# Performance work log

Measured on AMD Instinct MI355X. Metric: run time of the kernel, lower is better.

## Reference

```python
import jax, jax.numpy as jnp
import numpy as np

EMB = 1024
HEADS = 16
HEAD_DIM = EMB // HEADS


def setup_inputs() -> dict:
    key = jax.random.key(0)
    k1, k2, k3, k4 = jax.random.split(key, 4)
    x = jax.random.normal(k1, (4, 2048, EMB), dtype=jnp.float32)
    # torch Linear weight is [out, in]; store as [in, out] for x @ W
    W_qkv = jax.random.normal(k2, (EMB, 3 * EMB), dtype=jnp.float32) * (1.0 / np.sqrt(EMB))
    W_proj = jax.random.normal(k3, (EMB, EMB), dtype=jnp.float32) * (1.0 / np.sqrt(EMB))
    b_proj = jax.random.normal(k4, (EMB,), dtype=jnp.float32) * 0.01
    return {"x": x, "W_qkv": W_qkv, "W_proj": W_proj, "b_proj": b_proj}


def reference(x, W_qkv, W_proj, b_proj):
    B, S, D = x.shape
    H, hd = HEADS, HEAD_DIM
    qkv = x @ W_qkv                                  # [B,S,3D]
    q, k, v = jnp.split(qkv, 3, axis=-1)
    q = q.reshape(B, S, H, hd).transpose(0, 2, 1, 3)  # [B,H,S,hd]
    k = k.reshape(B, S, H, hd).transpose(0, 2, 1, 3)
    v = v.reshape(B, S, H, hd).transpose(0, 2, 1, 3)
    att = jnp.einsum('bhqd,bhkd->bhqk', q, k) * (1.0 / np.sqrt(hd))
    causal = jnp.tril(jnp.ones((S, S), dtype=bool))
    att = jnp.where(causal[None, None], att, jnp.float32(-jnp.inf))
    att = jax.nn.softmax(att, axis=-1)
    # dropout omitted (eval mode / deterministic baseline)
    out = jnp.einsum('bhqk,bhkd->bhqd', att, v)       # [B,H,S,hd]
    out = out.transpose(0, 2, 1, 3).reshape(B, S, D)
    return out @ W_proj + b_proj
```

## Files before the change

### kernel.cpp

```cpp
#include <hip/hip_runtime.h>
#include <math.h>

#define S_   2048
#define D_   1024
#define H_   16
#define HD_  64
#define BH_  64
#define TOK_ 8192

typedef __attribute__((ext_vector_type(8))) short  short8;
typedef __attribute__((ext_vector_type(4))) float  floatx4;

__device__ __forceinline__ short f2bf(float f) {
  union { float f; unsigned u; } c; c.f = f;
  unsigned u = c.u;
  u += 0x7fffu + ((u >> 16) & 1u);
  return (short)(u >> 16);
}

__device__ __forceinline__ float max3f(float a, float b, float c) {
  float d; asm("v_max3_f32 %0, %1, %2, %3" : "=v"(d) : "v"(a), "v"(b), "v"(c)); return d;
}

__device__ __forceinline__ void gload16(const void* g, void* l) {
  __builtin_amdgcn_global_load_lds((const __attribute__((address_space(1))) void*)g,
                                   (__attribute__((address_space(3))) void*)l, 16, 0, 0);
}

__global__ void cvt_x_kernel(const float* __restrict__ in, short* __restrict__ out, int n8) {
  int i = blockIdx.x * blockDim.x + threadIdx.x;
  if (i >= n8) return;
  const float4* p = (const float4*)in;
  float4 a = p[i * 2], b = p[i * 2 + 1];
  short8 o;
  o[0] = f2bf(a.x); o[1] = f2bf(a.y); o[2] = f2bf(a.z); o[3] = f2bf(a.w);
  o[4] = f2bf(b.x); o[5] = f2bf(b.y); o[6] = f2bf(b.z); o[7] = f2bf(b.w);
  ((short8*)out)[i] = o;
}

__global__ void tconv_kernel(const float* __restrict__ in, short* __restrict__ out, int R, int C) {
  __shared__ float t[32][33];
  int tx = threadIdx.x, ty = threadIdx.y;
  int c0 = blockIdx.x * 32, r0 = blockIdx.y * 32;
#pragma unroll
  for (int i = 0; i < 4; ++i)
    t[ty + i * 8][tx] = in[(r0 + ty + i * 8) * C + c0 + tx];
  __syncthreads();
#pragma unroll
  for (int i = 0; i < 4; ++i)
    out[(c0 + ty + i * 8) * R + r0 + tx] = f2bf(t[tx][ty + i * 8]);
}

__global__ __launch_bounds__(256) void gemm_qkv_kernel(
    const short* __restrict__ A, const short* __restrict__ Bt,
    short* __restrict__ qb, short* __restrict__ kb, short* __restrict__ vtb) {
  __shared__ short sA[128 * 32];
  __shared__ short sB[128 * 32];
  const int tid = threadIdx.x;
  const int lane = tid & 63, wid = tid >> 6;
  const int wm = wid >> 1, wn = wid & 1;
  const int lr = lane & 15, lg = lane >> 4;
  const int m0 = blockIdx.x * 128, n0 = blockIdx.y * 128;
  floatx4 acc[4][4] = {};
  const int f1 = tid * 16;
  const int rS1 = f1 >> 6, cS1 = (f1 & 63) >> 1;
  const int f2 = f1 + 4096;
  const int rS2 = f2 >> 6, cS2 = (f2 & 63) >> 1;
  for (int kt = 0; kt < 32; ++kt) {
    const int k0 = kt * 32;
    __syncthreads();
    gload16(&A[(m0 + rS1) * 1024 + k0 + cS1], (char*)sA + f1);
    gload16(&A[(m0 + rS2) * 1024 + k0 + cS2], (char*)sA + f2);
    gload16(&Bt[(n0 + rS1) * 1024 + k0 + cS1], (char*)sB + f1);
    gload16(&Bt[(n0 + rS2) * 1024 + k0 + cS2], (char*)sB + f2);
    __syncthreads();
    short8 af[4], bfv[4];
#pragma unroll
    for (int mf = 0; mf < 4; ++mf)
      af[mf] = *(const short8*)&sA[(wm * 64 + mf * 16 + lr) * 32 + lg * 8];
#pragma unroll
    for (int nf = 0; nf < 4; ++nf)
      bfv[nf] = *(const short8*)&sB[(wn * 64 + nf * 16 + lr) * 32 + lg * 8];
#pragma unroll
    for (int mf = 0; mf < 4; ++mf)
#pragma unroll
      for (int nf = 0; nf < 4; ++nf)
        acc[mf][nf] = __builtin_amdgcn_mfma_f32_16x16x32_bf16(af[mf], bfv[nf], acc[mf][nf], 0, 0, 0);
  }
  const int sec = n0 >> 10;
  if (sec < 2) {
    short* dst = sec == 0 ? qb : kb;
    const float scale = (sec == 0) ? 0.18033688011112042f : 1.0f;
#pragma unroll
    for (int mf = 0; mf < 4; ++mf) {
#pragma unroll
      for (int nf = 0; nf < 4; ++nf) {
        const int col = n0 + wn * 64 + nf * 16 + lr;
        const int w = col & 1023;
        const int h = w >> 6, d = w & 63;
#pragma unroll
        for (int r = 0; r < 4; ++r) {
          const int token = m0 + wm * 64 + mf * 16 + lg * 4 + r;
          const int b = token >> 11, s = token & 2047;
          dst[(((b << 4) | h) * 2048 + s) * 64 + d] = f2bf(acc[mf][nf][r] * scale);
        }
      }
    }
  } else {
#pragma unroll
    for (int mf = 0; mf < 4; ++mf) {
      const int token0 = m0 + wm * 64 + mf * 16 + lg * 4;
      const int bb = token0 >> 11, s0v = token0 & 2047;
#pragma unroll
      for (int nf = 0; nf < 4; ++nf) {
        const int col = n0 + wn * 64 + nf * 16 + lr;
        const int w = col & 1023;
        const int h = w >> 6, d = w & 63;
        union { unsigned long long u; short s[4]; } pk;
        pk.s[0] = f2bf(acc[mf][nf][0]);
        pk.s[1] = f2bf(acc[mf][nf][1]);
        pk.s[2] = f2bf(acc[mf][nf][2]);
        pk.s[3] = f2bf(acc[mf][nf][3]);
        *(unsigned long long*)&vtb[((((bb << 4) | h) * 64 + d) << 11) + s0v] = pk.u;
      }
    }
  }
}

__global__ __launch_bounds__(256) void gemm_proj_kernel(
    const short* __restrict__ A, const short* __restrict__ Bt,
    const float* __restrict__ bias, float* __restrict__ out) {
  __shared__ short sA[128 * 32];
  __shared__ short sB[128 * 32];
  const int tid = threadIdx.x;
  const int lane = tid & 63, wid = tid >> 6;
  const int wm = wid >> 1, wn = wid & 1;
  const int lr = lane & 15, lg = lane >> 4;
  const int m0 = blockIdx.x * 128, n0 = blockIdx.y * 128;
  floatx4 acc[4][4] = {};
  const int f1 = tid * 16;
  const int rS1 = f1 >> 6, cS1 = (f1 & 63) >> 1;
  const int f2 = f1 + 4096;
  const int rS2 = f2 >> 6, cS2 = (f2 & 63) >> 1;
  for (int kt = 0; kt < 32; ++kt) {
    const int k0 = kt * 32;
    __syncthreads();
    gload16(&A[(m0 + rS1) * 1024 + k0 + cS1], (char*)sA + f1);
    gload16(&A[(m0 + rS2) * 1024 + k0 + cS2], (char*)sA + f2);
    gload16(&Bt[(n0 + rS1) * 1024 + k0 + cS1], (char*)sB + f1);
    gload16(&Bt[(n0 + rS2) * 1024 + k0 + cS2], (char*)sB + f2);
    __syncthreads();
    short8 af[4], bfv[4];
#pragma unroll
    for (int mf = 0; mf < 4; ++mf)
      af[mf] = *(const short8*)&sA[(wm * 64 + mf * 16 + lr) * 32 + lg * 8];
#pragma unroll
    for (int nf = 0; nf < 4; ++nf)
      bfv[nf] = *(const short8*)&sB[(wn * 64 + nf * 16 + lr) * 32 + lg * 8];
#pragma unroll
    for (int mf = 0; mf < 4; ++mf)
#pragma unroll
      for (int nf = 0; nf < 4; ++nf)
        acc[mf][nf] = __builtin_amdgcn_mfma_f32_16x16x32_bf16(af[mf], bfv[nf], acc[mf][nf], 0, 0, 0);
  }
#pragma unroll
  for (int mf = 0; mf < 4; ++mf) {
#pragma unroll
    for (int nf = 0; nf < 4; ++nf) {
      const int col = n0 + wn * 64 + nf * 16 + lr;
      const float bv = bias[col];
#pragma unroll
      for (int r = 0; r < 4; ++r) {
        const int row = m0 + wm * 64 + mf * 16 + lg * 4 + r;
        out[row * 1024 + col] = acc[mf][nf][r] + bv;
      }
    }
  }
}

__global__ __launch_bounds__(256) void attn_kernel(
    const short* __restrict__ qb, const short* __restrict__ kb,
    const short* __restrict__ vtb, short* __restrict__ attb) {
  __shared__ short sK[3][64 * 64];
  __shared__ short sVT[3][64 * 64];
  __shared__ short sP[4][32 * 64];
  const int tid = threadIdx.x;
  const int lane = tid & 63, wid = tid >> 6;
  const int lr = lane & 15, lg = lane >> 4;

  const int bid = blockIdx.x;
  const int wgid = (bid & 7) * 64 + (bid >> 3);
  const int bh = wgid >> 3;
  const int qx = wgid & 7;

  const char* kbase = (const char*)(kb + bh * S_ * HD_);
  const char* vtbase = (const char*)(vtb + bh * HD_ * S_);
  const short* qbase = qb + bh * S_ * HD_;
  char* pbase = (char*)&sP[wid][0];
  const int b = bh >> 4, h = bh & 15;

  const int f1 = tid * 16;
  const int ro1 = f1 >> 7, cb1 = f1 & 127;
  const int sc1 = cb1 ^ ((ro1 & 7) << 4);
  const int f2 = f1 + 4096;
  const int ro2 = f2 >> 7, cb2 = f2 & 127;
  const int sc2 = cb2 ^ ((ro2 & 7) << 4);

  const int swz = (lr & 7) << 4;

  short8 vones;
#pragma unroll
  for (int j = 0; j < 8; ++j) vones[j] = (short)0x3F80;

#pragma unroll 1
  for (int half = 0; half < 2; ++half) {
    const int qt = half ? (15 - qx) : qx;
    const int qw = qt * 128 + wid * 32;

    short8 qf[2][2];
#pragma unroll
    for (int qtile = 0; qtile < 2; ++qtile)
#pragma unroll
      for (int kf = 0; kf < 2; ++kf)
        qf[qtile][kf] = *(const short8*)&qbase[(qw + qtile * 16 + lr) * 64 + kf * 32 + lg * 8];

    floatx4 acc_o[2][4] = {};
    floatx4 acc_den[2] = {};
    float mrun[2] = {-1e30f, -1e30f};

    const int ntiles = 2 * qt + 2;

    __builtin_amdgcn_s_barrier();

    const char* kp1 = kbase + ro1 * 128 + sc1;
    const char* kp2 = kbase + ro2 * 128 + sc2;
    const char* vp1 = vtbase + ro1 * 4096 + sc1;
    const char* vp2 = vtbase + ro2 * 4096 + sc2;

    gload16(kp1, (char*)sK[0] + f1);  gload16(kp2, (char*)sK[0] + f2);
    gload16(vp1, (char*)sVT[0] + f1); gload16(vp2, (char*)sVT[0] + f2);
    kp1 += 8192; kp2 += 8192; vp1 += 128; vp2 += 128;
    gload16(kp1, (char*)sK[1] + f1);  gload16(kp2, (char*)sK[1] + f2);
    gload16(vp1, (char*)sVT[1] + f1); gload16(vp2, (char*)sVT[1] + f2);
    kp1 += 8192; kp2 += 8192; vp1 += 128; vp2 += 128;

    int cur = 0, nxt2 = 2;
#pragma unroll 1
    for (int t = 0; t < ntiles; ++t) {
      if (t < ntiles - 1) { asm volatile("s_waitcnt vmcnt(4)" ::: "memory"); }
      else                { asm volatile("s_waitcnt vmcnt(0)" ::: "memory"); }
      __builtin_amdgcn_s_barrier();
      __builtin_amdgcn_sched_barrier(0);
      if (t + 2 < ntiles) {
        char* dK = (char*)sK[nxt2];
        char* dV = (char*)sVT[nxt2];
        gload16(kp1, dK + f1);  gload16(kp2, dK + f2);
        gload16(vp1, dV + f1);  gload16(vp2, dV + f2);
      }
      kp1 += 8192; kp2 += 8192; vp1 += 128; vp2 += 128;

      const int key0 = t * 64;
      if (key0 <= qw + 31) {
        const char* cK = (const char*)sK[cur];
        const char* cV = (const char*)sVT[cur];

        floatx4 sT[4][2] = {};
        __builtin_amdgcn_s_setprio(1);
#pragma unroll
        for (int kt = 0; kt < 4; ++kt) {
#pragma unroll
          for (int kf = 0; kf < 2; ++kf) {
            short8 kfrag = *(const short8*)(cK + (kt * 16 + lr) * 128 + ((kf * 64 + lg * 16) ^ swz));
#pragma unroll
            for (int qtile = 0; qtile < 2; ++qtile)
              sT[kt][qtile] = __builtin_amdgcn_mfma_f32_16x16x32_bf16(kfrag, qf[qtile][kf], sT[kt][qtile], 0, 0, 0);
          }
        }
        __builtin_amdgcn_s_setprio(0);

        if (key0 + 63 > qw) {
#pragma unroll
          for (int kt = 0; kt < 4; ++kt)
#pragma unroll
            for (int qtile = 0; qtile < 2; ++qtile)
#pragma unroll
              for (int r = 0; r < 4; ++r)
                if (key0 + kt * 16 + lg * 4 + r > qw + qtile * 16 + lr) sT[kt][qtile][r] = -1e30f;
        }

        float mx[2], al[2];
        bool need = false;
#pragma unroll
        for (int qtile = 0; qtile < 2; ++qtile) {
          float m = max3f(sT[0][qtile][0], sT[0][qtile][1], sT[0][qtile][2]);
          m = max3f(m, sT[0][qtile][3], sT[1][qtile][0]);
          m = max3f(m, sT[1][qtile][1], sT[1][qtile][2]);
          m = max3f(m, sT[1][qtile][3], sT[2][qtile][0]);
          m = max3f(m, sT[2][qtile][1], sT[2][qtile][2]);
          m = max3f(m, sT[2][qtile][3], sT[3][qtile][0]);
          m = max3f(m, sT[3][qtile][1], sT[3][qtile][2]);
          m = fmaxf(m, sT[3][qtile][3]);
          m = fmaxf(m, __shfl_xor(m, 16));
          m = fmaxf(m, __shfl_xor(m, 32));
          mx[qtile] = m;
          need = need || (m > mrun[qtile] + 8.f);
        }
        if (__any(need)) {
#pragma unroll
          for (int qtile = 0; qtile < 2; ++qtile) {
            const float mnew = fmaxf(mrun[qtile], mx[qtile]);
            al[qtile] = __builtin_amdgcn_exp2f(mrun[qtile] - mnew);
            mrun[qtile] = mnew;
          }
#pragma unroll
          for (int mf = 0; mf < 2; ++mf) {
#pragma unroll
            for (int r = 0; r < 4; ++r) {
              const float alr = __shfl(al[mf], lg * 4 + r);
              acc_den[mf][r] *= alr;
#pragma unroll
              for (int nfd = 0; nfd < 4; ++nfd) acc_o[mf][nfd][r] *= alr;
            }
          }
        }

#pragma unroll
        for (int kt = 0; kt < 4; ++kt) {
#pragma unroll
          for (int qtile = 0; qtile < 2; ++qtile) {
            const float p0 = __builtin_amdgcn_exp2f(sT[kt][qtile][0] - mrun[qtile]);
            const float p1 = __builtin_amdgcn_exp2f(sT[kt][qtile][1] - mrun[qtile]);
            const float p2 = __builtin_amdgcn_exp2f(sT[kt][qtile][2] - mrun[qtile]);
            const float p3 = __builtin_amdgcn_exp2f(sT[kt][qtile][3] - mrun[qtile]);
            unsigned lo, hi;
            asm("v_cvt_pk_bf16_f32 %0, %1, %2" : "=v"(lo) : "v"(p0), "v"(p1));
            asm("v_cvt_pk_bf16_f32 %0, %1, %2" : "=v"(hi) : "v"(p2), "v"(p3));
            *(unsigned long long*)(pbase + (qtile * 16 + lr) * 128 + ((kt * 32 + lg * 8) ^ swz)) =
                ((unsigned long long)hi << 32) | lo;
          }
        }

        __builtin_amdgcn_s_setprio(1);
#pragma unroll
        for (int kf2 = 0; kf2 < 2; ++kf2) {
          short8 pf[2];
#pragma unroll
          for (int mf = 0; mf < 2; ++mf) {
            pf[mf] = *(const short8*)(pbase + (mf * 16 + lr) * 128 + ((kf2 * 64 + lg * 16) ^ swz));
            acc_den[mf] = __builtin_amdgcn_mfma_f32_16x16x32_bf16(pf[mf], vones, acc_den[mf], 0, 0, 0);
          }
#pragma unroll
          for (int nfd = 0; nfd < 4; ++nfd) {
            short8 vfrag = *(const short8*)(cV + (nfd * 16 + lr) * 128 + ((kf2 * 64 + lg * 16) ^ swz));
#pragma unroll
            for (int mf = 0; mf < 2; ++mf)
              acc_o[mf][nfd] = __builtin_amdgcn_mfma_f32_16x16x32_bf16(pf[mf], vfrag, acc_o[mf][nfd], 0, 0, 0);
          }
        }
        __builtin_amdgcn_s_setprio(0);
      }

      cur = (cur == 2) ? 0 : cur + 1;
      nxt2 = (nxt2 == 2) ? 0 : nxt2 + 1;
    }

#pragma unroll
    for (int mf = 0; mf < 2; ++mf) {
#pragma unroll
      for (int nfd = 0; nfd < 4; ++nfd) {
#pragma unroll
        for (int r = 0; r < 4; ++r) {
          const float o = acc_o[mf][nfd][r] / acc_den[mf][r];
          const int qrow = qw + mf * 16 + lg * 4 + r;
          const int d = nfd * 16 + lr;
          attb[(b * 2048 + qrow) * 1024 + h * 64 + d] = f2bf(o);
        }
      }
    }
  }
}

extern "C" void kernel_launch(void* const* d_in, const int* in_sizes, int n_in,
                              void* d_out, int out_size, void* d_ws, size_t ws_size,
                              hipStream_t stream) {
  (void)in_sizes; (void)n_in; (void)out_size; (void)ws_size;
  const float* x = (const float*)d_in[0];
  const float* Wqkv = (const float*)d_in[1];
  const float* Wproj = (const float*)d_in[2];
  const float* bproj = (const float*)d_in[3];
  float* out = (float*)d_out;

  char* w = (char*)d_ws;
  short* xb     = (short*)(w + 0);
  short* wqkvT  = (short*)(w + 16777216);
  short* wprojT = (short*)(w + 23068672);
  short* qb     = (short*)(w + 25165824);
  short* kb     = (short*)(w + 41943040);
  short* vtb    = (short*)(w + 75497472);
  short* attb   = (short*)(w + 92274688);

  cvt_x_kernel<<<4096, 256, 0, stream>>>(x, xb, TOK_ * D_ / 8);
  tconv_kernel<<<dim3(96, 32), dim3(32, 8), 0, stream>>>(Wqkv, wqkvT, 1024, 3072);
  tconv_kernel<<<dim3(32, 32), dim3(32, 8), 0, stream>>>(Wproj, wprojT, 1024, 1024);
  gemm_qkv_kernel<<<dim3(64, 24), 256, 0, stream>>>(xb, wqkvT, qb, kb, vtb);
  attn_kernel<<<512, 256, 0, stream>>>(qb, kb, vtb, attb);
  gemm_proj_kernel<<<dim3(64, 8), 256, 0, stream>>>(attb, wprojT, bproj, out);
}
```

Measured before the change: 264.7 us.

## Double-buffer LDS tiles in QKV and projection GEMMs to overlap loads with MFMA

```diff
diff --git a/kernel.cpp b/kernel.cpp
--- a/kernel.cpp
+++ b/kernel.cpp
@@ -54,8 +54,8 @@
 __global__ __launch_bounds__(256) void gemm_qkv_kernel(
     const short* __restrict__ A, const short* __restrict__ Bt,
     short* __restrict__ qb, short* __restrict__ kb, short* __restrict__ vtb) {
-  __shared__ short sA[128 * 32];
-  __shared__ short sB[128 * 32];
+  __shared__ short sA[2][128 * 32];
+  __shared__ short sB[2][128 * 32];
   const int tid = threadIdx.x;
   const int lane = tid & 63, wid = tid >> 6;
   const int wm = wid >> 1, wn = wid & 1;
@@ -66,27 +66,47 @@
   const int rS1 = f1 >> 6, cS1 = (f1 & 63) >> 1;
   const int f2 = f1 + 4096;
   const int rS2 = f2 >> 6, cS2 = (f2 & 63) >> 1;
+  const short* Ab1 = &A[(m0 + rS1) * 1024 + cS1];
+  const short* Ab2 = &A[(m0 + rS2) * 1024 + cS2];
+  const short* Bb1 = &Bt[(n0 + rS1) * 1024 + cS1];
+  const short* Bb2 = &Bt[(n0 + rS2) * 1024 + cS2];
+
+  gload16(Ab1, (char*)sA[0] + f1);
+  gload16(Ab2, (char*)sA[0] + f2);
+  gload16(Bb1, (char*)sB[0] + f1);
+  gload16(Bb2, (char*)sB[0] + f2);
+  asm volatile("s_waitcnt vmcnt(0)" ::: "memory");
+  __builtin_amdgcn_s_barrier();
+  __builtin_amdgcn_sched_barrier(0);
+
+  int cur = 0;
   for (int kt = 0; kt < 32; ++kt) {
-    const int k0 = kt * 32;
-    __syncthreads();
-    gload16(&A[(m0 + rS1) * 1024 + k0 + cS1], (char*)sA + f1);
-    gload16(&A[(m0 + rS2) * 1024 + k0 + cS2], (char*)sA + f2);
-    gload16(&Bt[(n0 + rS1) * 1024 + k0 + cS1], (char*)sB + f1);
-    gload16(&Bt[(n0 + rS2) * 1024 + k0 + cS2], (char*)sB + f2);
-    __syncthreads();
+    if (kt < 31) {
+      const int k0n = (kt + 1) * 32;
+      gload16(Ab1 + k0n, (char*)sA[cur ^ 1] + f1);
+      gload16(Ab2 + k0n, (char*)sA[cur ^ 1] + f2);
+      gload16(Bb1 + k0n, (char*)sB[cur ^ 1] + f1);
+      gload16(Bb2 + k0n, (char*)sB[cur ^ 1] + f2);
+    }
     short8 af[4], bfv[4];
 #pragma unroll
     for (int mf = 0; mf < 4; ++mf)
-      af[mf] = *(const short8*)&sA[(wm * 64 + mf * 16 + lr) * 32 + lg * 8];
+      af[mf] = *(const short8*)&sA[cur][(wm * 64 + mf * 16 + lr) * 32 + lg * 8];
 #pragma unroll
     for (int nf = 0; nf < 4; ++nf)
-      bfv[nf] = *(const short8*)&sB[(wn * 64 + nf * 16 + lr) * 32 + lg * 8];
+      bfv[nf] = *(const short8*)&sB[cur][(wn * 64 + nf * 16 + lr) * 32 + lg * 8];
 #pragma unroll
     for (int mf = 0; mf < 4; ++mf)
 #pragma unroll
       for (int nf = 0; nf < 4; ++nf)
         acc[mf][nf] = __builtin_amdgcn_mfma_f32_16x16x32_bf16(af[mf], bfv[nf], acc[mf][nf], 0, 0, 0);
+    __builtin_amdgcn_sched_barrier(0);
+    asm volatile("s_waitcnt vmcnt(0)" ::: "memory");
+    __builtin_amdgcn_s_barrier();
+    __builtin_amdgcn_sched_barrier(0);
+    cur ^= 1;
   }
+
   const int sec = n0 >> 10;
   if (sec < 2) {
     short* dst = sec == 0 ? qb : kb;
@@ -130,8 +150,8 @@
 __global__ __launch_bounds__(256) void gemm_proj_kernel(
     const short* __restrict__ A, const short* __restrict__ Bt,
     const float* __restrict__ bias, float* __restrict__ out) {
-  __shared__ short sA[128 * 32];
-  __shared__ short sB[128 * 32];
+  __shared__ short sA[2][128 * 32];
+  __shared__ short sB[2][128 * 32];
   const int tid = threadIdx.x;
   const int lane = tid & 63, wid = tid >> 6;
   const int wm = wid >> 1, wn = wid & 1;
@@ -142,26 +162,45 @@
   const int rS1 = f1 >> 6, cS1 = (f1 & 63) >> 1;
   const int f2 = f1 + 4096;
   const int rS2 = f2 >> 6, cS2 = (f2 & 63) >> 1;
+  const short* Ab1 = &A[(m0 + rS1) * 1024 + cS1];
+  const short* Ab2 = &A[(m0 + rS2) * 1024 + cS2];
+  const short* Bb1 = &Bt[(n0 + rS1) * 1024 + cS1];
+  const short* Bb2 = &Bt[(n0 + rS2) * 1024 + cS2];
+
+  gload16(Ab1, (char*)sA[0] + f1);
+  gload16(Ab2, (char*)sA[0] + f2);
+  gload16(Bb1, (char*)sB[0] + f1);
+  gload16(Bb2, (char*)sB[0] + f2);
+  asm volatile("s_waitcnt vmcnt(0)" ::: "memory");
+  __builtin_amdgcn_s_barrier();
+  __builtin_amdgcn_sched_barrier(0);
+
+  int cur = 0;
   for (int kt = 0; kt < 32; ++kt) {
-    const int k0 = kt * 32;
-    __syncthreads();
-    gload16(&A[(m0 + rS1) * 1024 + k0 + cS1], (char*)sA + f1);
-    gload16(&A[(m0 + rS2) * 1024 + k0 + cS2], (char*)sA + f2);
-    gload16(&Bt[(n0 + rS1) * 1024 + k0 + cS1], (char*)sB + f1);
-    gload16(&Bt[(n0 + rS2) * 1024 + k0 + cS2], (char*)sB + f2);
-    __syncthreads();
+    if (kt < 31) {
+      const int k0n = (kt + 1) * 32;
+      gload16(Ab1 + k0n, (char*)sA[cur ^ 1] + f1);
+      gload16(Ab2 + k0n, (char*)sA[cur ^ 1] + f2);
+      gload16(Bb1 + k0n, (char*)sB[cur ^ 1] + f1);
+      gload16(Bb2 + k0n, (char*)sB[cur ^ 1] + f2);
+    }
     short8 af[4], bfv[4];
 #pragma unroll
     for (int mf = 0; mf < 4; ++mf)
-      af[mf] = *(const short8*)&sA[(wm * 64 + mf * 16 + lr) * 32 + lg * 8];
+      af[mf] = *(const short8*)&sA[cur][(wm * 64 + mf * 16 + lr) * 32 + lg * 8];
 #pragma unroll
     for (int nf = 0; nf < 4; ++nf)
-      bfv[nf] = *(const short8*)&sB[(wn * 64 + nf * 16 + lr) * 32 + lg * 8];
+      bfv[nf] = *(const short8*)&sB[cur][(wn * 64 + nf * 16 + lr) * 32 + lg * 8];
 #pragma unroll
     for (int mf = 0; mf < 4; ++mf)
 #pragma unroll
       for (int nf = 0; nf < 4; ++nf)
         acc[mf][nf] = __builtin_amdgcn_mfma_f32_16x16x32_bf16(af[mf], bfv[nf], acc[mf][nf], 0, 0, 0);
+    __builtin_amdgcn_sched_barrier(0);
+    asm volatile("s_waitcnt vmcnt(0)" ::: "memory");
+    __builtin_amdgcn_s_barrier();
+    __builtin_amdgcn_sched_barrier(0);
+    cur ^= 1;
   }
 #pragma unroll
   for (int mf = 0; mf < 4; ++mf) {
```

After: 268.2 us. About the same (+1.3%).
